# Performance work log

Measured on AMD Instinct MI355X. Metric: run time of the kernel, lower is better.

Reference implementation:

```python
import jax, jax.numpy as jnp
import numpy as np

N_ITER = 5  # Newton-Schulz iterations (matches n_iter default in source)


def _isqrt_newton_schulz_batch(A, num_iters):
    # A: [B, C, C] SPD matrices -> A^{-1/2} via coupled Newton-Schulz,
    # exactly mirroring isqrt_newton_schulz_autograd_batch in the source.
    b, dim, _ = A.shape
    normA = jnp.sqrt(jnp.sum(A * A, axis=(1, 2), keepdims=True))  # Frobenius norm per batch
    Y = A / normA
    I = jnp.broadcast_to(jnp.eye(dim, dtype=A.dtype), A.shape)
    Z = I
    for _ in range(num_iters):
        T = 0.5 * (3.0 * I - Z @ Y)
        Y = Y @ T
        Z = T @ Z
    return Z / jnp.sqrt(normA)


def setup_inputs() -> dict:
    key = jax.random.key(0)
    k1, k2, k3 = jax.random.split(key, 3)
    B, C, H, W = 8, 256, 128, 128
    r = 8  # reduction
    x = jax.random.normal(k1, (B, C, H, W), dtype=jnp.float32)
    w1 = jax.random.normal(k2, (C // r, C), dtype=jnp.float32) * 0.05  # squeeze 1x1 conv
    b1 = jnp.zeros((C // r,), dtype=jnp.float32)
    w2 = jax.random.normal(k3, (C, C // r), dtype=jnp.float32) * 0.05  # excite 1x1 conv
    b2 = jnp.zeros((C,), dtype=jnp.float32)
    return {"x": x, "w1": w1, "b1": b1, "w2": w2, "b2": b2}


def reference(x, w1, b1, w2, b2):
    B, C, H, W = x.shape
    M = H * W
    # global second-order (covariance) pooling
    xf = x.reshape(B, C, M)
    xc = xf - jnp.mean(xf, axis=-1, keepdims=True)          # center over spatial dim
    cov = jnp.einsum('bcm,bdm->bcd', xc, xc) / M            # [B, C, C]
    A_isqrt = _isqrt_newton_schulz_batch(cov, N_ITER)       # [B, C, C]
    # channel statistic: row mean of the matrix-(inverse-)sqrt
    y = jnp.mean(A_isqrt, axis=-1)                          # [B, C]
    # squeeze-excite gating (1x1 convs == dense over channels)
    h = jax.nn.relu(y @ w1.T + b1)                          # [B, C//r]
    g = jax.nn.sigmoid(h @ w2.T + b2)                       # [B, C]
    return x * g[:, :, None, None]
```

## Files before the change

kernel.cpp:

```cpp
#include <hip/hip_runtime.h>
#include <cstdint>
#include <cstddef>

typedef short s8vec __attribute__((ext_vector_type(8)));
typedef float f16acc __attribute__((ext_vector_type(16)));

#define C_DIM 256
#define M_DIM 16384
#define BATCH 8
#define KSPLIT 32
#define KCHUNK 512
#define BK 64
#define LDSP 72

static __device__ __forceinline__ unsigned short f2bf(float f) {
    union { float f; unsigned u; } v; v.f = f;
    unsigned r = v.u + 0x7fffu + ((v.u >> 16) & 1u);
    return (unsigned short)(r >> 16);
}
static __device__ __forceinline__ float bf2f(unsigned short h) {
    union { unsigned u; float f; } v; v.u = ((unsigned)h) << 16;
    return v.f;
}

__global__ __launch_bounds__(256, 2)
void cov_kernel(const float* __restrict__ x, float* __restrict__ covraw,
                float* __restrict__ sums)
{
    __shared__ unsigned short As[128][LDSP];
    __shared__ unsigned short Bs[128][LDSP];
    const int tile = blockIdx.x;
    const int kc   = blockIdx.y;
    const int b    = blockIdx.z;
    const int trow = (tile == 0) ? 0 : 128;
    const int tcol = (tile == 2) ? 0 : trow;
    const bool diag = (tile < 2);

    const int tid  = threadIdx.x;
    const int lane = tid & 63;
    const int wave = tid >> 6;
    const int wr = wave >> 1, wc = wave & 1;
    const int half = lane >> 5, l31 = lane & 31;

    const float* xb = x + (size_t)b * C_DIM * M_DIM + (size_t)kc * KCHUNK;

    f16acc acc[2][2] = {};
    float rowsum[8] = {0,0,0,0,0,0,0,0};
    const int sr = tid >> 4;
    const int sc = (tid & 15) * 4;

    float4 va[8], vb[8];
    {
        const float* sa = xb + (size_t)(trow + sr) * M_DIM + sc;
        #pragma unroll
        for (int i = 0; i < 8; ++i)
            va[i] = *(const float4*)(sa + (size_t)(16 * i) * M_DIM);
        if (!diag) {
            const float* sb2 = xb + (size_t)(tcol + sr) * M_DIM + sc;
            #pragma unroll
            for (int i = 0; i < 8; ++i)
                vb[i] = *(const float4*)(sb2 + (size_t)(16 * i) * M_DIM);
        }
    }

    const unsigned short (*Bp)[LDSP] = diag ? As : Bs;

    for (int kt = 0; kt < KCHUNK / BK; ++kt) {
        __syncthreads();
        #pragma unroll
        for (int i = 0; i < 8; ++i) {
            if (diag) rowsum[i] += va[i].x + va[i].y + va[i].z + va[i].w;
            ushort4 p;
            p.x = f2bf(va[i].x); p.y = f2bf(va[i].y);
            p.z = f2bf(va[i].z); p.w = f2bf(va[i].w);
            *(ushort4*)&As[sr + 16 * i][sc] = p;
        }
        if (!diag) {
            #pragma unroll
            for (int i = 0; i < 8; ++i) {
                ushort4 p;
                p.x = f2bf(vb[i].x); p.y = f2bf(vb[i].y);
                p.z = f2bf(vb[i].z); p.w = f2bf(vb[i].w);
                *(ushort4*)&Bs[sr + 16 * i][sc] = p;
            }
        }
        if (kt < KCHUNK / BK - 1) {
            const float* sa = xb + (size_t)(trow + sr) * M_DIM + (kt + 1) * BK + sc;
            #pragma unroll
            for (int i = 0; i < 8; ++i)
                va[i] = *(const float4*)(sa + (size_t)(16 * i) * M_DIM);
            if (!diag) {
                const float* sb2 = xb + (size_t)(tcol + sr) * M_DIM + (kt + 1) * BK + sc;
                #pragma unroll
                for (int i = 0; i < 8; ++i)
                    vb[i] = *(const float4*)(sb2 + (size_t)(16 * i) * M_DIM);
            }
        }
        __syncthreads();
        #pragma unroll
        for (int ks = 0; ks < 4; ++ks) {
            const int k0 = ks * 16 + half * 8;
            s8vec af[2], bfr[2];
            #pragma unroll
            for (int i = 0; i < 2; ++i)
                af[i] = *(const s8vec*)&As[wr * 64 + i * 32 + l31][k0];
            #pragma unroll
            for (int j = 0; j < 2; ++j)
                bfr[j] = *(const s8vec*)&Bp[wc * 64 + j * 32 + l31][k0];
            #pragma unroll
            for (int i = 0; i < 2; ++i)
                #pragma unroll
                for (int j = 0; j < 2; ++j)
                    acc[i][j] = __builtin_amdgcn_mfma_f32_32x32x16_bf16(
                        af[i], bfr[j], acc[i][j], 0, 0, 0);
        }
    }
    if (diag) {
        #pragma unroll
        for (int i = 0; i < 8; ++i) {
            float s = rowsum[i];
            s += __shfl_down(s, 8, 16);
            s += __shfl_down(s, 4, 16);
            s += __shfl_down(s, 2, 16);
            s += __shfl_down(s, 1, 16);
            if ((lane & 15) == 0)
                atomicAdd(&sums[b * C_DIM + trow + sr + 16 * i], s);
        }
    }
    float* covb = covraw + (size_t)b * C_DIM * C_DIM;
    #pragma unroll
    for (int i = 0; i < 2; ++i) {
        const int rb = trow + wr * 64 + i * 32 + 4 * half;
        #pragma unroll
        for (int j = 0; j < 2; ++j) {
            const int cb = tcol + wc * 64 + j * 32 + l31;
            #pragma unroll
            for (int r = 0; r < 16; ++r) {
                const int row = rb + (r & 3) + 8 * (r >> 2);
                atomicAdd(&covb[row * C_DIM + cb], acc[i][j][r]);
            }
        }
    }
}

__global__ __launch_bounds__(256)
void cov_normsq(const float* __restrict__ covraw, const float* __restrict__ sums,
                float* __restrict__ normsq)
{
    const int slab = blockIdx.x;
    const int b    = blockIdx.y;
    const int tid  = threadIdx.x;
    const float invM = 1.0f / (float)M_DIM;
    const float* cb = covraw + (size_t)b * 65536;
    const float* sb = sums + b * 256;
    float ss = 0.0f;
    #pragma unroll 4
    for (int i = 0; i < 32; ++i) {
        const int e = slab * 8192 + i * 256 + tid;
        const int r = e >> 8, c = e & 255;
        const float raw = (r < 128 && c >= 128) ? cb[c * 256 + r] : cb[e];
        const float v = raw * invM - (sb[r] * invM) * (sb[c] * invM);
        ss += v * v;
    }
    #pragma unroll
    for (int off = 32; off; off >>= 1) ss += __shfl_down(ss, off, 64);
    __shared__ float red[4];
    if ((tid & 63) == 0) red[tid >> 6] = ss;
    __syncthreads();
    if (tid == 0)
        atomicAdd(&normsq[b], red[0] + red[1] + red[2] + red[3]);
}

__global__ __launch_bounds__(256)
void emit_YT(const float* __restrict__ covraw, const float* __restrict__ sums,
             const float* __restrict__ normsq, float* __restrict__ normA_g,
             unsigned short* __restrict__ Y0, unsigned short* __restrict__ T0)
{
    const int slab = blockIdx.x;
    const int b    = blockIdx.y;
    const int tid  = threadIdx.x;
    const float invM = 1.0f / (float)M_DIM;
    const float nq  = normsq[b];
    const float inv = rsqrtf(nq);
    if (slab == 0 && tid == 0) normA_g[b] = sqrtf(nq);
    const float* cb = covraw + (size_t)b * 65536;
    const float* sb = sums + b * 256;
    unsigned short* yb = Y0 + (size_t)b * 65536;
    unsigned short* tb = T0 + (size_t)b * 65536;
    #pragma unroll 4
    for (int i = 0; i < 32; ++i) {
        const int e = slab * 8192 + i * 256 + tid;
        const int r = e >> 8, c = e & 255;
        const float raw = (r < 128 && c >= 128) ? cb[c * 256 + r] : cb[e];
        const float v = (raw * invM - (sb[r] * invM) * (sb[c] * invM)) * inv;
        yb[e] = f2bf(v);
        tb[e] = f2bf(((r == c) ? 1.5f : 0.0f) - 0.5f * v);
    }
}

__global__ __launch_bounds__(256, 4)
void ns_stage(const unsigned short* __restrict__ A0, const unsigned short* __restrict__ B0,
              unsigned short* __restrict__ C0,
              const unsigned short* __restrict__ A1, const unsigned short* __restrict__ B1,
              unsigned short* __restrict__ C1,
              float c0, float c1)
{
    __shared__ unsigned short As[64][LDSP];
    __shared__ unsigned short Bs[64][LDSP];
    const int b = blockIdx.y;
    const int trow = (blockIdx.x >> 2) * 64, tcol = (blockIdx.x & 3) * 64;
    const unsigned short* A = (blockIdx.z ? A1 : A0) + (size_t)b * 65536;
    const unsigned short* B = (blockIdx.z ? B1 : B0) + (size_t)b * 65536;
    unsigned short* Cp = (blockIdx.z ? C1 : C0) + (size_t)b * 65536;

    const int tid = threadIdx.x;
    const int lane = tid & 63, wave = tid >> 6;
    const int wr = wave >> 1, wc = wave & 1;
    const int half = lane >> 5, l31 = lane & 31;

    f16acc acc = {};

    const int sr = tid >> 3;
    const int sc = (tid & 7) * 8;
    for (int kt = 0; kt < 4; ++kt) {
        const int kb = kt * BK;
        uint4 va[2], vb[2];
        #pragma unroll
        for (int i = 0; i < 2; ++i) {
            va[i] = *(const uint4*)(A + (size_t)(trow + sr + 32 * i) * 256 + kb + sc);
            vb[i] = *(const uint4*)(B + (size_t)(tcol + sr + 32 * i) * 256 + kb + sc);
        }
        __syncthreads();
        #pragma unroll
        for (int i = 0; i < 2; ++i) {
            *(uint4*)&As[sr + 32 * i][sc] = va[i];
            *(uint4*)&Bs[sr + 32 * i][sc] = vb[i];
        }
        __syncthreads();
        #pragma unroll
        for (int ks = 0; ks < 4; ++ks) {
            const int k0 = ks * 16 + half * 8;
            s8vec af = *(const s8vec*)&As[wr * 32 + l31][k0];
            s8vec bfr = *(const s8vec*)&Bs[wc * 32 + l31][k0];
            acc = __builtin_amdgcn_mfma_f32_32x32x16_bf16(af, bfr, acc, 0, 0, 0);
        }
    }
    const int rb = trow + wr * 32 + 4 * half;
    const int cb = tcol + wc * 32 + l31;
    #pragma unroll
    for (int r = 0; r < 16; ++r) {
        const int row = rb + (r & 3) + 8 * (r >> 2);
        float v = c1 * acc[r] + ((row == cb) ? c0 : 0.0f);
        Cp[row * 256 + cb] = f2bf(v);
    }
}

__global__ __launch_bounds__(256)
void gating_kernel(const unsigned short* __restrict__ Zfin, const float* __restrict__ normA_g,
                   const float* __restrict__ w1, const float* __restrict__ b1,
                   const float* __restrict__ w2, const float* __restrict__ b2,
                   float* __restrict__ g)
{
    const int b = blockIdx.x;
    const int tid = threadIdx.x;
    __shared__ float sy[256];
    __shared__ float sh[32];
    const unsigned short* zr = Zfin + (size_t)b * 65536 + (size_t)tid * 256;
    float s = 0.0f;
    #pragma unroll
    for (int i = 0; i < 32; ++i) {
        uint4 v = *(const uint4*)(zr + i * 8);
        const unsigned short* p = (const unsigned short*)&v;
        #pragma unroll
        for (int j = 0; j < 8; ++j) s += bf2f(p[j]);
    }
    const float scale = (1.0f / 256.0f) / sqrtf(normA_g[b]);
    sy[tid] = s * scale;
    __syncthreads();
    if (tid < 32) {
        float hh = b1[tid];
        const float* w1r = w1 + tid * 256;
        for (int c = 0; c < 256; ++c) hh += w1r[c] * sy[c];
        sh[tid] = hh > 0.0f ? hh : 0.0f;
    }
    __syncthreads();
    float z = b2[tid];
    const float* w2r = w2 + tid * 32;
    #pragma unroll
    for (int j = 0; j < 32; ++j) z += w2r[j] * sh[j];
    g[b * 256 + tid] = 1.0f / (1.0f + expf(-z));
}

__global__ __launch_bounds__(256)
void scale_kernel(const float* __restrict__ x, const float* __restrict__ g,
                  float* __restrict__ out)
{
    const float4* x4 = (const float4*)x;
    float4* o4 = (float4*)out;
    #pragma unroll
    for (int it = 0; it < 4; ++it) {
        size_t i = (size_t)blockIdx.x * 1024 + it * 256 + threadIdx.x;
        float gg = g[i >> 12];
        float4 v = x4[i];
        float4 r;
        r.x = v.x * gg; r.y = v.y * gg; r.z = v.z * gg; r.w = v.w * gg;
        o4[i] = r;
    }
}

extern "C" void kernel_launch(void* const* d_in, const int* in_sizes, int n_in,
                              void* d_out, int out_size, void* d_ws, size_t ws_size,
                              hipStream_t stream)
{
    const float* x  = (const float*)d_in[0];
    const float* w1 = (const float*)d_in[1];
    const float* b1 = (const float*)d_in[2];
    const float* w2 = (const float*)d_in[3];
    const float* b2 = (const float*)d_in[4];
    float* out = (float*)d_out;

    char* ws = (char*)d_ws;
    float* covraw = (float*)ws;
    float* sums   = (float*)(ws + 2097152);
    float* normsq = (float*)(ws + 2105344);
    float* normA  = (float*)(ws + 2105600);
    float* g      = (float*)(ws + 2106368);
    unsigned short* Ya = (unsigned short*)(ws + 4194304);
    unsigned short* Yb = (unsigned short*)(ws + 5242880);
    unsigned short* Za = (unsigned short*)(ws + 6291456);
    unsigned short* Zb = (unsigned short*)(ws + 7340032);
    unsigned short* T  = (unsigned short*)(ws + 8388608);

    hipMemsetAsync(covraw, 0, 2105408, stream);

    cov_kernel<<<dim3(3, KSPLIT, BATCH), 256, 0, stream>>>(x, covraw, sums);
    cov_normsq<<<dim3(8, BATCH), 256, 0, stream>>>(covraw, sums, normsq);
    emit_YT<<<dim3(8, BATCH), 256, 0, stream>>>(covraw, sums, normsq, normA, Ya, Za);

    ns_stage<<<dim3(16, BATCH, 1), 256, 0, stream>>>(Ya, Za, Yb, Ya, Za, Yb, 0.0f, 1.0f);

    unsigned short* Ycur = Yb; unsigned short* Yoth = Ya;
    unsigned short* Zcur = Za; unsigned short* Zoth = Zb;
    for (int it = 0; it < 4; ++it) {
        ns_stage<<<dim3(16, BATCH, 1), 256, 0, stream>>>(
            Zcur, Ycur, T, Zcur, Ycur, T, 1.5f, -0.5f);
        if (it < 3) {
            ns_stage<<<dim3(16, BATCH, 2), 256, 0, stream>>>(
                Ycur, T, Yoth, T, Zcur, Zoth, 0.0f, 1.0f);
            unsigned short* t0 = Ycur; Ycur = Yoth; Yoth = t0;
            unsigned short* t1 = Zcur; Zcur = Zoth; Zoth = t1;
        } else {
            ns_stage<<<dim3(16, BATCH, 1), 256, 0, stream>>>(
                T, Zcur, Zoth, T, Zcur, Zoth, 0.0f, 1.0f);
            Zcur = Zoth;
        }
    }
    gating_kernel<<<BATCH, 256, 0, stream>>>(Zcur, normA, w1, b1, w2, b2, g);
    scale_kernel<<<8192, 256, 0, stream>>>(x, g, out);
}
```

Measured before the change: 387.3 us.

## Replace late Newton-Schulz matmuls with matrix-vector chains applied to ones vector

Only the final row mean of Z is needed, i.e. Z·1, so the last Newton-Schulz iterations are no longer formed as full 256x256 matrix products. They are applied implicitly as chains of matrix-vector products inside the gating kernel, using the iterate-2 Y and Z matrices. This drops most of the ns_stage launches and their bf16 matmul traffic. The change also merges the normsq and emit kernels into one 1024-thread kernel per batch, which removes the normsq atomic, and raises cov_kernel's occupancy hint. In exchange the gating kernel becomes a long serial chain of synchronised matvecs on only 8 blocks.

```diff
diff --git a/kernel.cpp b/kernel.cpp
--- a/kernel.cpp
+++ b/kernel.cpp
@@ -23,7 +23,7 @@
     return v.f;
 }
 
-__global__ __launch_bounds__(256, 2)
+__global__ __launch_bounds__(256, 4)
 void cov_kernel(const float* __restrict__ x, float* __restrict__ covraw,
                 float* __restrict__ sums)
 {
@@ -143,20 +143,23 @@
     }
 }
 
-__global__ __launch_bounds__(256)
-void cov_normsq(const float* __restrict__ covraw, const float* __restrict__ sums,
-                float* __restrict__ normsq)
-{
-    const int slab = blockIdx.x;
-    const int b    = blockIdx.y;
-    const int tid  = threadIdx.x;
+__global__ __launch_bounds__(1024)
+void normsq_emit(const float* __restrict__ covraw, const float* __restrict__ sums,
+                 float* __restrict__ normA_g,
+                 unsigned short* __restrict__ Y0, unsigned short* __restrict__ T0)
+{
+    const int b = blockIdx.x;
+    const int tid = threadIdx.x;
     const float invM = 1.0f / (float)M_DIM;
     const float* cb = covraw + (size_t)b * 65536;
     const float* sb = sums + b * 256;
+    __shared__ float red[16];
+    __shared__ float stot;
+
     float ss = 0.0f;
     #pragma unroll 4
-    for (int i = 0; i < 32; ++i) {
-        const int e = slab * 8192 + i * 256 + tid;
+    for (int i = 0; i < 64; ++i) {
+        const int e = i * 1024 + tid;
         const int r = e >> 8, c = e & 255;
         const float raw = (r < 128 && c >= 128) ? cb[c * 256 + r] : cb[e];
         const float v = raw * invM - (sb[r] * invM) * (sb[c] * invM);
@@ -164,32 +167,22 @@
     }
     #pragma unroll
     for (int off = 32; off; off >>= 1) ss += __shfl_down(ss, off, 64);
-    __shared__ float red[4];
     if ((tid & 63) == 0) red[tid >> 6] = ss;
     __syncthreads();
-    if (tid == 0)
-        atomicAdd(&normsq[b], red[0] + red[1] + red[2] + red[3]);
-}
-
-__global__ __launch_bounds__(256)
-void emit_YT(const float* __restrict__ covraw, const float* __restrict__ sums,
-             const float* __restrict__ normsq, float* __restrict__ normA_g,
-             unsigned short* __restrict__ Y0, unsigned short* __restrict__ T0)
-{
-    const int slab = blockIdx.x;
-    const int b    = blockIdx.y;
-    const int tid  = threadIdx.x;
-    const float invM = 1.0f / (float)M_DIM;
-    const float nq  = normsq[b];
-    const float inv = rsqrtf(nq);
-    if (slab == 0 && tid == 0) normA_g[b] = sqrtf(nq);
-    const float* cb = covraw + (size_t)b * 65536;
-    const float* sb = sums + b * 256;
+    if (tid == 0) {
+        float t = 0.0f;
+        #pragma unroll
+        for (int i = 0; i < 16; ++i) t += red[i];
+        stot = t;
+        normA_g[b] = sqrtf(t);
+    }
+    __syncthreads();
+    const float inv = rsqrtf(stot);
     unsigned short* yb = Y0 + (size_t)b * 65536;
     unsigned short* tb = T0 + (size_t)b * 65536;
     #pragma unroll 4
-    for (int i = 0; i < 32; ++i) {
-        const int e = slab * 8192 + i * 256 + tid;
+    for (int i = 0; i < 64; ++i) {
+        const int e = i * 1024 + tid;
         const int r = e >> 8, c = e & 255;
         const float raw = (r < 128 && c >= 128) ? cb[c * 256 + r] : cb[e];
         const float v = (raw * invM - (sb[r] * invM) * (sb[c] * invM)) * inv;
@@ -255,32 +248,69 @@
     }
 }
 
+static __device__ __forceinline__ float mv256(const unsigned short* __restrict__ M,
+                                              float xval, float* xs, int tid)
+{
+    xs[tid] = xval;
+    __syncthreads();
+    const unsigned short* mr = M + (size_t)tid * 256;
+    float acc = 0.0f;
+    #pragma unroll 4
+    for (int i = 0; i < 32; ++i) {
+        uint4 v = *(const uint4*)(mr + i * 8);
+        const unsigned short* p = (const unsigned short*)&v;
+        #pragma unroll
+        for (int j = 0; j < 8; ++j) acc += bf2f(p[j]) * xs[i * 8 + j];
+    }
+    __syncthreads();
+    return acc;
+}
+
+struct MVCtx { const unsigned short* Y; const unsigned short* Z; float* xs; int tid; };
+
+static __device__ __forceinline__ float T2ap(const MVCtx& m, float u) {
+    float p = mv256(m.Y, u, m.xs, m.tid);
+    float q = mv256(m.Z, p, m.xs, m.tid);
+    return 1.5f * u - 0.5f * q;
+}
+static __device__ __forceinline__ float Y3ap(const MVCtx& m, float u) {
+    return mv256(m.Y, T2ap(m, u), m.xs, m.tid);
+}
+static __device__ __forceinline__ float Z3ap(const MVCtx& m, float u) {
+    return T2ap(m, mv256(m.Z, u, m.xs, m.tid));
+}
+static __device__ __forceinline__ float T3ap(const MVCtx& m, float u) {
+    float w = Z3ap(m, Y3ap(m, u));
+    return 1.5f * u - 0.5f * w;
+}
+
 __global__ __launch_bounds__(256)
-void gating_kernel(const unsigned short* __restrict__ Zfin, const float* __restrict__ normA_g,
+void gating_kernel(const unsigned short* __restrict__ Y2, const unsigned short* __restrict__ Z2,
+                   const float* __restrict__ normA_g,
                    const float* __restrict__ w1, const float* __restrict__ b1,
                    const float* __restrict__ w2, const float* __restrict__ b2,
                    float* __restrict__ g)
 {
     const int b = blockIdx.x;
     const int tid = threadIdx.x;
-    __shared__ float sy[256];
+    __shared__ float xs[256];
     __shared__ float sh[32];
-    const unsigned short* zr = Zfin + (size_t)b * 65536 + (size_t)tid * 256;
-    float s = 0.0f;
-    #pragma unroll
-    for (int i = 0; i < 32; ++i) {
-        uint4 v = *(const uint4*)(zr + i * 8);
-        const unsigned short* p = (const unsigned short*)&v;
-        #pragma unroll
-        for (int j = 0; j < 8; ++j) s += bf2f(p[j]);
-    }
-    const float scale = (1.0f / 256.0f) / sqrtf(normA_g[b]);
-    sy[tid] = s * scale;
+    MVCtx m { Y2 + (size_t)b * 65536, Z2 + (size_t)b * 65536, xs, tid };
+
+    float s  = Z3ap(m, 1.0f);
+    float a  = T3ap(m, s);
+    float bv = T3ap(m, a);
+    float c  = Y3ap(m, bv);
+    float d  = Z3ap(m, c);
+    float e  = T3ap(m, d);
+
+    const float y = (1.5f * a - 0.5f * e) * (1.0f / 256.0f) / sqrtf(normA_g[b]);
+    xs[tid] = y;
     __syncthreads();
     if (tid < 32) {
         float hh = b1[tid];
         const float* w1r = w1 + tid * 256;
-        for (int c = 0; c < 256; ++c) hh += w1r[c] * sy[c];
+        for (int c2 = 0; c2 < 256; ++c2) hh += w1r[c2] * xs[c2];
         sh[tid] = hh > 0.0f ? hh : 0.0f;
     }
     __syncthreads();
@@ -322,39 +352,24 @@
     char* ws = (char*)d_ws;
     float* covraw = (float*)ws;
     float* sums   = (float*)(ws + 2097152);
-    float* normsq = (float*)(ws + 2105344);
     float* normA  = (float*)(ws + 2105600);
     float* g      = (float*)(ws + 2106368);
     unsigned short* Ya = (unsigned short*)(ws + 4194304);
     unsigned short* Yb = (unsigned short*)(ws + 5242880);
     unsigned short* Za = (unsigned short*)(ws + 6291456);
     unsigned short* Zb = (unsigned short*)(ws + 7340032);
-    unsigned short* T  = (unsigned short*)(ws + 8388608);
-
-    hipMemsetAsync(covraw, 0, 2105408, stream);
+    unsigned short* Tm = (unsigned short*)(ws + 8388608);
+
+    hipMemsetAsync(covraw, 0, 2105344, stream);
 
     cov_kernel<<<dim3(3, KSPLIT, BATCH), 256, 0, stream>>>(x, covraw, sums);
-    cov_normsq<<<dim3(8, BATCH), 256, 0, stream>>>(covraw, sums, normsq);
-    emit_YT<<<dim3(8, BATCH), 256, 0, stream>>>(covraw, sums, normsq, normA, Ya, Za);
+
+    normsq_emit<<<BATCH, 1024, 0, stream>>>(covraw, sums, normA, Ya, Za);
 
     ns_stage<<<dim3(16, BATCH, 1), 256, 0, stream>>>(Ya, Za, Yb, Ya, Za, Yb, 0.0f, 1.0f);
-
-    unsigned short* Ycur = Yb; unsigned short* Yoth = Ya;
-    unsigned short* Zcur = Za; unsigned short* Zoth = Zb;
-    for (int it = 0; it < 4; ++it) {
-        ns_stage<<<dim3(16, BATCH, 1), 256, 0, stream>>>(
-            Zcur, Ycur, T, Zcur, Ycur, T, 1.5f, -0.5f);
-        if (it < 3) {
-            ns_stage<<<dim3(16, BATCH, 2), 256, 0, stream>>>(
-                Ycur, T, Yoth, T, Zcur, Zoth, 0.0f, 1.0f);
-            unsigned short* t0 = Ycur; Ycur = Yoth; Yoth = t0;
-            unsigned short* t1 = Zcur; Zcur = Zoth; Zoth = t1;
-        } else {
-            ns_stage<<<dim3(16, BATCH, 1), 256, 0, stream>>>(
-                T, Zcur, Zoth, T, Zcur, Zoth, 0.0f, 1.0f);
-            Zcur = Zoth;
-        }
-    }
-    gating_kernel<<<BATCH, 256, 0, stream>>>(Zcur, normA, w1, b1, w2, b2, g);
+    ns_stage<<<dim3(16, BATCH, 1), 256, 0, stream>>>(Za, Yb, Tm, Za, Yb, Tm, 1.5f, -0.5f);
+    ns_stage<<<dim3(16, BATCH, 2), 256, 0, stream>>>(Yb, Tm, Ya, Tm, Za, Zb, 0.0f, 1.0f);
+
+    gating_kernel<<<BATCH, 256, 0, stream>>>(Ya, Zb, normA, w1, b1, w2, b2, g);
     scale_kernel<<<8192, 256, 0, stream>>>(x, g, out);
 }
```

After: 591.2 us. 1.53x slower.
